# Kernel tuning notes

Measured on AMD Instinct MI355X. Metric: run time of the kernel, lower is better.

## Reference

```python
import jax, jax.numpy as jnp
import numpy as np

T, B, F, H = 128, 64, 75, 512
J = F  # attention dim == number of input features (joints)


def _lstm_dir(x, h0, c0, Wih, Whh, bih, bhh, reverse):
    # x: (T,B,Fin). Precompute input projection once (big GEMM), scan the recurrence.
    xw = jnp.einsum('tbf,gf->tbg', x, Wih) + bih + bhh  # (T,B,4H)

    def step(carry, xt):
        h, c = carry
        g = xt + h @ Whh.T  # (B,4H), PyTorch gate order i,f,g,o
        i, f, gg, o = jnp.split(g, 4, axis=-1)
        c = jax.nn.sigmoid(f) * c + jax.nn.sigmoid(i) * jnp.tanh(gg)
        h = jax.nn.sigmoid(o) * jnp.tanh(c)
        return (h, c), h

    (hT, cT), ys = jax.lax.scan(step, (h0, c0), xw, reverse=reverse)
    return ys, hT


def _bilstm(x, h0, c0, Wih, Whh, bih, bhh):
    # params have leading direction axis of size 2
    yf, hf = _lstm_dir(x, h0[0], c0[0], Wih[0], Whh[0], bih[0], bhh[0], False)
    yb, hb = _lstm_dir(x, h0[1], c0[1], Wih[1], Whh[1], bih[1], bhh[1], True)
    return jnp.concatenate([yf, yb], axis=-1), jnp.stack([hf, hb])


def setup_inputs() -> dict:
    key = jax.random.key(0)
    ks = iter(jax.random.split(key, 40))

    def p(*shape):
        return (jax.random.normal(next(ks), shape, dtype=jnp.float32) * 0.05)

    inp = {
        'x': jax.random.normal(next(ks), (T, B, F), dtype=jnp.float32),
        'h0': jnp.zeros((6, B, H), jnp.float32),
        'c0': jnp.zeros((6, B, H), jnp.float32),
        # salstm: 1-layer bidirectional, input F
        'sa_Wih': p(2, 4 * H, F), 'sa_Whh': p(2, 4 * H, H),
        'sa_bih': p(2, 4 * H), 'sa_bhh': p(2, 4 * H),
        # mainlstm layer 0 (input F)
        'm0_Wih': p(2, 4 * H, F), 'm0_Whh': p(2, 4 * H, H),
        'm0_bih': p(2, 4 * H), 'm0_bhh': p(2, 4 * H),
        # mainlstm layers 1,2 (input 2H), stacked on leading layer axis
        'mL_Wih': p(2, 2, 4 * H, 2 * H), 'mL_Whh': p(2, 2, 4 * H, H),
        'mL_bih': p(2, 2, 4 * H), 'mL_bhh': p(2, 2, 4 * H),
        'safc1_W': p(H, H), 'safc1_b': p(H),
        'safc2_W': p(J, H), 'safc2_b': p(J),
        'fc1_W': p(H, 2 * H), 'fc1_b': p(H),
    }
    return inp


def reference(x, h0, c0, sa_Wih, sa_Whh, sa_bih, sa_bhh,
              m0_Wih, m0_Whh, m0_bih, m0_bhh,
              mL_Wih, mL_Whh, mL_bih, mL_bhh,
              safc1_W, safc1_b, safc2_W, safc2_b, fc1_W, fc1_b):
    # spatial-attention LSTM
    sa_out, sa_hn = _bilstm(x, h0[:2], c0[:2], sa_Wih, sa_Whh, sa_bih, sa_bhh)  # sa_hn (2,B,H)
    e = jnp.exp(jnp.tanh(sa_hn @ safc1_W.T + safc1_b) @ safc2_W.T + safc2_b)  # (2,B,J)
    alpha = e / e.sum(axis=(0, 2), keepdims=True)  # per-batch normalization
    # replace all weights >= 0.1 with their selected mean (per batch element)
    mask = alpha >= 0.1
    cnt = mask.sum(axis=(0, 2), keepdims=True)
    sel_mean = (alpha * mask).sum(axis=(0, 2), keepdims=True) / jnp.maximum(cnt, 1)
    alpha = jnp.where(mask, sel_mean, alpha)
    alpha_b = alpha.mean(axis=0)  # (B,J) -- reconcile direction axis for broadcast

    xw = x * alpha_b[None]  # (T,B,F)

    # 3-layer bidirectional main LSTM
    y, _ = _bilstm(xw, h0[0:2], c0[0:2], m0_Wih, m0_Whh, m0_bih, m0_bhh)
    for l in range(2):
        y, _ = _bilstm(y, h0[2 + 2 * l:4 + 2 * l], c0[2 + 2 * l:4 + 2 * l],
                       mL_Wih[l], mL_Whh[l], mL_bih[l], mL_bhh[l])
    out = y @ fc1_W.T + fc1_b  # (T,B,H)
    return out
```

## Files before the change

### kernel.cpp

```cpp
#include <hip/hip_runtime.h>
#include <cstddef>

#define T_  128
#define B_  64
#define F_  75
#define H_  512
#define G4_ 2048
#define TB_ (T_ * B_)
#define KP_ 128

typedef __bf16 bf16x8 __attribute__((ext_vector_type(8)));
typedef float  f32x4  __attribute__((ext_vector_type(4)));
typedef unsigned long long u64;

__device__ __forceinline__ short f2b(float x) {
    union { float f; unsigned u; } v; v.f = x;
    return (short)((v.u + 0x7fffu + ((v.u >> 16) & 1u)) >> 16);
}
__device__ __forceinline__ float b2f(short s) {
    union { float f; unsigned u; } v; v.u = ((unsigned)(unsigned short)s) << 16;
    return v.f;
}
__device__ __forceinline__ void gload16(const void* g, void* l) {
    __builtin_amdgcn_global_load_lds(
        (const __attribute__((address_space(1))) void*)g,
        (__attribute__((address_space(3))) void*)l, 16, 0, 0);
}
__device__ __forceinline__ float fsig(float x) {
    return __builtin_amdgcn_rcpf(1.f + __expf(-x));
}
__device__ __forceinline__ float ftanh(float x) {
    return 1.f - 2.f * __builtin_amdgcn_rcpf(1.f + __expf(2.f * x));
}

__global__ __launch_bounds__(256) void gemm_bf16(
    const short* __restrict__ A, const short* __restrict__ Bm,
    float* __restrict__ C, float* __restrict__ P, int M, int N, int K,
    const float* __restrict__ bias1, const float* __restrict__ bias2)
{
    __shared__ short As[4096];
    __shared__ short Bs[4096];
    const int tid = threadIdx.x;
    const int m_base = blockIdx.y * 128;
    const int n_base = blockIdx.x * 128;
    const int w = tid >> 6, lane = tid & 63;
    const int wm = (w >> 1) * 64, wn = (w & 1) * 64;
    const int lm = lane & 15, q = lane >> 4;

    f32x4 acc[4][4];
#pragma unroll
    for (int i = 0; i < 4; i++)
#pragma unroll
        for (int j = 0; j < 4; j++)
#pragma unroll
            for (int r = 0; r < 4; r++) acc[i][j][r] = 0.f;

    const int s0 = tid, s1 = tid + 256;
    const int r0 = s0 & 127, c0 = s0 >> 7;
    const int r1 = s1 & 127, c1 = s1 >> 7;

    for (int k0 = 0; k0 < K; k0 += 32) {
        __syncthreads();
        gload16(A + (size_t)(m_base + r0) * K + k0 + c0 * 8, &As[s0 * 8]);
        gload16(A + (size_t)(m_base + r1) * K + k0 + c1 * 8, &As[s1 * 8]);
        gload16(Bm + (size_t)(n_base + r0) * K + k0 + c0 * 8, &Bs[s0 * 8]);
        gload16(Bm + (size_t)(n_base + r1) * K + k0 + c1 * 8, &Bs[s1 * 8]);
        __syncthreads();
        bf16x8 af[4], bfv[4];
#pragma unroll
        for (int i = 0; i < 4; i++) {
            af[i]  = *(const bf16x8*)&As[((q * 128) + wm + i * 16 + lm) * 8];
            bfv[i] = *(const bf16x8*)&Bs[((q * 128) + wn + i * 16 + lm) * 8];
        }
#pragma unroll
        for (int i = 0; i < 4; i++)
#pragma unroll
            for (int j = 0; j < 4; j++)
                acc[i][j] = __builtin_amdgcn_mfma_f32_16x16x32_bf16(
                    af[i], bfv[j], acc[i][j], 0, 0, 0);
    }

#pragma unroll
    for (int i = 0; i < 4; i++) {
#pragma unroll
        for (int j = 0; j < 4; j++) {
            const int gm0 = m_base + wm + i * 16 + q * 4;
            const int gn = n_base + wn + j * 16 + lm;
            float bb = (bias1 ? bias1[gn] : 0.f) + (bias2 ? bias2[gn] : 0.f);
            if (P) {
                const int g = gn >> 9, u = gn & 511;
                const int ub = u >> 4, lmu = u & 15;
#pragma unroll
                for (int r = 0; r < 4; r++) {
                    const int gm = gm0 + r;
                    const int t = gm >> 6, b = gm & 63;
                    const int tidS = (b >> 4) * 64 + ((b >> 2) & 3) * 16 + lmu;
                    size_t idx = ((((size_t)t * 32 + ub) * 4 + (b & 3)) * 256 + tidS) * 4 + g;
                    P[idx] = acc[i][j][r] + bb;
                }
            } else {
#pragma unroll
                for (int r = 0; r < 4; r++)
                    C[(size_t)(gm0 + r) * N + gn] = acc[i][j][r] + bb;
            }
        }
    }
}

__global__ __launch_bounds__(256) void pack_whh(
    const float* __restrict__ W, short* __restrict__ Wpk)
{
    int i = blockIdx.x * 256 + threadIdx.x;
    if (i >= 2 * G4_ * H_) return;
    int e = i & 7, lane = (i >> 3) & 63, it = (i >> 9) & 15;
    int g = (i >> 13) & 3, ub = (i >> 15) & 31, dir = (i >> 20) & 1;
    int lm = lane & 15, qq = lane >> 4;
    float v = W[((size_t)dir * G4_ + g * H_ + ub * 16 + lm) * H_
                + it * 32 + qq * 8 + e];
    Wpk[i] = f2b(v);
}

__global__ __launch_bounds__(256) void init_phase(
    const float* __restrict__ h0s, short* __restrict__ Ht,
    unsigned* __restrict__ bar, int zero_bar)
{
    int i = blockIdx.x * 256 + threadIdx.x;
    if (i < 2 * B_ * H_) Ht[i] = f2b(h0s[i]);
    if (zero_bar && i < 64) bar[i] = 0;
}

__global__ __launch_bounds__(256) void ht_to_f32(
    const short* __restrict__ Ht0, float* __restrict__ out)
{
    int i = blockIdx.x * 256 + threadIdx.x;
    if (i < 2 * B_ * H_) out[i] = b2f(Ht0[i]);
}

__global__ __launch_bounds__(256, 1) void lstm_phase(
    const float* __restrict__ XW,
    const short* __restrict__ Wpk,
    short* __restrict__ Ht,
    const float* __restrict__ c0p,
    short* __restrict__ Y,
    unsigned* __restrict__ bar, int phase)
{
    __shared__ short Ws[32768];
    __shared__ short Tb[64 * 24];
    const int dir = blockIdx.y, ub = blockIdx.x, u0 = ub * 16;
    const int tid = threadIdx.x, w = tid >> 6, lane = tid & 63;
    const int lm = lane & 15, q = lane >> 4;

    const short* wsrc = Wpk + (size_t)(dir * 32 + ub) * 32768;
#pragma unroll
    for (int p = 0; p < 16; p++)
        gload16(wsrc + (tid + 256 * p) * 8, &Ws[(tid + 256 * p) * 8]);

    const int b0 = w * 16 + q * 4;
    const int u = u0 + lm;
    unsigned* slots = bar + dir * 32;

    float c[4];
    f32x4 xw[4];
#pragma unroll
    for (int r = 0; r < 4; r++)
        c[r] = c0p[(size_t)dir * B_ * H_ + (size_t)(b0 + r) * H_ + u];
    {
        const int t0 = dir ? (T_ - 1) : 0;
        const float* xp = XW + ((size_t)dir * T_ + t0) * (B_ * G4_) + (size_t)ub * 4096;
#pragma unroll
        for (int r = 0; r < 4; r++)
            xw[r] = *(const f32x4*)(xp + r * 1024 + tid * 4);
    }
    __syncthreads();

    for (int s = 0; s < T_; s++) {
        const int t = dir ? (T_ - 1 - s) : s;
        const short* Hc = Ht + ((size_t)((s & 1) * 2 + dir) << 15);

        u64 hq[32];
#pragma unroll
        for (int it = 0; it < 16; it++) {
            const u64* hp = (const u64*)(Hc + (w * 16 + lm) * 512 + it * 32 + q * 8);
            hq[2 * it]     = __hip_atomic_load((u64*)hp,     __ATOMIC_RELAXED, __HIP_MEMORY_SCOPE_AGENT);
            hq[2 * it + 1] = __hip_atomic_load((u64*)hp + 1, __ATOMIC_RELAXED, __HIP_MEMORY_SCOPE_AGENT);
        }

        f32x4 acc[4];
#pragma unroll
        for (int g = 0; g < 4; g++)
#pragma unroll
            for (int r = 0; r < 4; r++) acc[g][r] = 0.f;

#pragma unroll
        for (int it = 0; it < 16; it++) {
            union { u64 q2[2]; bf16x8 v; } ua;
            ua.q2[0] = hq[2 * it]; ua.q2[1] = hq[2 * it + 1];
#pragma unroll
            for (int g = 0; g < 4; g++) {
                bf16x8 bv = *(const bf16x8*)&Ws[((g * 16 + it) * 64 + lane) * 8];
                acc[g] = __builtin_amdgcn_mfma_f32_16x16x32_bf16(ua.v, bv, acc[g], 0, 0, 0);
            }
        }

#pragma unroll
        for (int r = 0; r < 4; r++) {
            float gi = acc[0][r] + xw[r][0];
            float gf = acc[1][r] + xw[r][1];
            float gg = acc[2][r] + xw[r][2];
            float go = acc[3][r] + xw[r][3];
            float cc = fsig(gf) * c[r] + fsig(gi) * ftanh(gg);
            c[r] = cc;
            Tb[(b0 + r) * 24 + lm] = f2b(fsig(go) * ftanh(cc));
        }
        __syncthreads();

        {
            const int b = tid >> 2, qd = tid & 3;
            u64 v0 = *(const u64*)&Tb[b * 24 + qd * 4];
            short* Hn = Ht + ((size_t)(((s + 1) & 1) * 2 + dir) << 15);
            __hip_atomic_store((u64*)(Hn + b * 512 + u0 + qd * 4), v0,
                               __ATOMIC_RELAXED, __HIP_MEMORY_SCOPE_AGENT);
            if (Y)
                *(u64*)(Y + ((size_t)t * B_ + b) * (2 * H_) + dir * H_ + u0 + qd * 4) = v0;
        }
        __asm__ volatile("s_waitcnt vmcnt(0)" ::: "memory");

        const unsigned tgt4 = (unsigned)(phase * T_ + s + 1) * 4u;
        if (lane == 0)
            __hip_atomic_fetch_add(&slots[ub], 1u, __ATOMIC_RELAXED, __HIP_MEMORY_SCOPE_AGENT);

        if (s < T_ - 1) {
            const int tn = dir ? (T_ - 2 - s) : (s + 1);
            const float* xp = XW + ((size_t)dir * T_ + tn) * (B_ * G4_) + (size_t)ub * 4096;
#pragma unroll
            for (int r = 0; r < 4; r++)
                xw[r] = *(const f32x4*)(xp + r * 1024 + tid * 4);
        }

        unsigned v;
        do {
            __builtin_amdgcn_s_sleep(1);
            v = (lane < 32)
                ? __hip_atomic_load(&slots[lane], __ATOMIC_RELAXED, __HIP_MEMORY_SCOPE_AGENT)
                : tgt4;
        } while (__any(v < tgt4));
        __syncthreads();
    }
}

__global__ __launch_bounds__(256) void gemm_bt(
    const float* __restrict__ A, const float* __restrict__ Bm,
    float* __restrict__ C, int M, int N, int K,
    const float* __restrict__ bias1, int act)
{
    __shared__ float As[16][68];
    __shared__ float Bs[16][68];
    const int tid = threadIdx.x;
    const int m_base = blockIdx.y * 64;
    const int n_base = blockIdx.x * 64;
    const int tm = tid >> 4, tn = tid & 15;
    float acc[4][4] = {};

    for (int k0 = 0; k0 < K; k0 += 16) {
#pragma unroll
        for (int i = 0; i < 4; i++) {
            int idx = tid * 4 + i;
            int r = idx >> 4, kk = idx & 15;
            int gm = m_base + r, gk = k0 + kk;
            As[kk][r] = (gm < M && gk < K) ? A[(size_t)gm * K + gk] : 0.f;
            int gn = n_base + r;
            Bs[kk][r] = (gn < N && gk < K) ? Bm[(size_t)gn * K + gk] : 0.f;
        }
        __syncthreads();
#pragma unroll
        for (int kk = 0; kk < 16; kk++) {
            float4 av = *(const float4*)&As[kk][tm * 4];
            float4 bv = *(const float4*)&Bs[kk][tn * 4];
            float a[4] = {av.x, av.y, av.z, av.w};
            float b[4] = {bv.x, bv.y, bv.z, bv.w};
#pragma unroll
            for (int i = 0; i < 4; i++)
#pragma unroll
                for (int j = 0; j < 4; j++)
                    acc[i][j] = fmaf(a[i], b[j], acc[i][j]);
        }
        __syncthreads();
    }
#pragma unroll
    for (int i = 0; i < 4; i++) {
        int gm = m_base + tm * 4 + i;
        if (gm >= M) continue;
#pragma unroll
        for (int j = 0; j < 4; j++) {
            int gn = n_base + tn * 4 + j;
            if (gn >= N) continue;
            float v = acc[i][j];
            if (bias1) v += bias1[gn];
            if (act == 1) v = tanhf(v);
            else if (act == 2) v = expf(v);
            C[(size_t)gm * N + gn] = v;
        }
    }
}

__global__ __launch_bounds__(256) void conv_f2b(
    const float* __restrict__ src, short* __restrict__ dst, int n)
{
    int i = blockIdx.x * 256 + threadIdx.x;
    if (i < n) dst[i] = f2b(src[i]);
}
__global__ __launch_bounds__(256) void conv_f2b_pad(
    const float* __restrict__ src, short* __restrict__ dst,
    int rows, int kin, int kp)
{
    int i = blockIdx.x * 256 + threadIdx.x;
    if (i < rows * kp) {
        int r = i / kp, k = i % kp;
        dst[i] = (k < kin) ? f2b(src[(size_t)r * kin + k]) : (short)0;
    }
}

__global__ __launch_bounds__(256) void attn_alpha(
    const float* __restrict__ E, float* __restrict__ AB)
{
    const int b = blockIdx.x, tid = threadIdx.x;
    __shared__ float red[256];
    __shared__ float adj[152];
    float v = 0.f;
    if (tid < 150) {
        int d = tid / F_, j = tid % F_;
        v = E[((size_t)d * B_ + b) * F_ + j];
    }
    red[tid] = v; __syncthreads();
    for (int s2 = 128; s2 > 0; s2 >>= 1) {
        if (tid < s2) red[tid] += red[tid + s2];
        __syncthreads();
    }
    float total = red[0]; __syncthreads();
    float alpha = v / total;
    float m = (tid < 150 && alpha >= 0.1f) ? 1.f : 0.f;
    red[tid] = m; __syncthreads();
    for (int s2 = 128; s2 > 0; s2 >>= 1) {
        if (tid < s2) red[tid] += red[tid + s2];
        __syncthreads();
    }
    float cnt = red[0]; __syncthreads();
    red[tid] = m * alpha; __syncthreads();
    for (int s2 = 128; s2 > 0; s2 >>= 1) {
        if (tid < s2) red[tid] += red[tid + s2];
        __syncthreads();
    }
    float selsum = red[0]; __syncthreads();
    float selmean = selsum / fmaxf(cnt, 1.f);
    if (tid < 150) adj[tid] = (m > 0.f) ? selmean : alpha;
    __syncthreads();
    if (tid < F_) AB[(size_t)b * F_ + tid] = 0.5f * (adj[tid] + adj[F_ + tid]);
}

__global__ __launch_bounds__(256) void scale_xb(
    const float* __restrict__ x, const float* __restrict__ AB,
    short* __restrict__ xb)
{
    int i = blockIdx.x * 256 + threadIdx.x;
    if (i < TB_ * KP_) {
        int r = i >> 7, k = i & 127;
        if (k < F_) {
            int b = r % B_;
            xb[i] = f2b(x[(size_t)r * F_ + k] * AB[(size_t)b * F_ + k]);
        } else xb[i] = 0;
    }
}

extern "C" void kernel_launch(void* const* d_in, const int* in_sizes, int n_in,
                              void* d_out, int out_size, void* d_ws, size_t ws_size,
                              hipStream_t stream)
{
    (void)in_sizes; (void)n_in; (void)out_size; (void)ws_size;
    const float* x       = (const float*)d_in[0];
    const float* h0      = (const float*)d_in[1];
    const float* c0      = (const float*)d_in[2];
    const float* sa_Wih  = (const float*)d_in[3];
    const float* sa_Whh  = (const float*)d_in[4];
    const float* sa_bih  = (const float*)d_in[5];
    const float* sa_bhh  = (const float*)d_in[6];
    const float* m0_Wih  = (const float*)d_in[7];
    const float* m0_Whh  = (const float*)d_in[8];
    const float* m0_bih  = (const float*)d_in[9];
    const float* m0_bhh  = (const float*)d_in[10];
    const float* mL_Wih  = (const float*)d_in[11];
    const float* mL_Whh  = (const float*)d_in[12];
    const float* mL_bih  = (const float*)d_in[13];
    const float* mL_bhh  = (const float*)d_in[14];
    const float* safc1_W = (const float*)d_in[15];
    const float* safc1_b = (const float*)d_in[16];
    const float* safc2_W = (const float*)d_in[17];
    const float* safc2_b = (const float*)d_in[18];
    const float* fc1_W   = (const float*)d_in[19];
    const float* fc1_b   = (const float*)d_in[20];

    char* cur = (char*)d_ws;
    auto alloc = [&](size_t bytes) {
        char* p = cur; cur += (bytes + 255) & ~(size_t)255; return p;
    };
    float*    XW   = (float*)alloc((size_t)2 * TB_ * G4_ * 4);
    float*    T1b  = (float*)alloc(2 * B_ * H_ * 4);
    float*    Eb   = (float*)alloc(2 * B_ * F_ * 4);
    float*    AB   = (float*)alloc(B_ * F_ * 4);
    float*    saHf = (float*)alloc(2 * B_ * H_ * 4);
    short*    xb   = (short*)alloc((size_t)TB_ * KP_ * 2);
    short*    Y0b  = (short*)alloc((size_t)TB_ * 2 * H_ * 2);
    short*    Y1b  = (short*)alloc((size_t)TB_ * 2 * H_ * 2);
    short*    Ht   = (short*)alloc((size_t)2 * 2 * B_ * H_ * 2);
    short*    Wpk  = (short*)alloc((size_t)2 * G4_ * H_ * 2);
    short*    Wihb = (short*)alloc((size_t)2 * G4_ * KP_ * 2);
    short*    WihbL= (short*)alloc((size_t)2 * G4_ * 2 * H_ * 2);
    short*    fc1b = (short*)alloc((size_t)H_ * 2 * H_ * 2);
    unsigned* bar  = (unsigned*)alloc(256);

    auto cv = [&](const float* s, short* d, int n) {
        conv_f2b<<<(n + 255) / 256, 256, 0, stream>>>(s, d, n);
    };
    auto g16 = [&](const short* Ap, const short* Bp, float* Cp, float* Pp,
                   int M, int N, int K, const float* b1, const float* b2) {
        gemm_bf16<<<dim3(N / 128, M / 128), 256, 0, stream>>>(Ap, Bp, Cp, Pp, M, N, K, b1, b2);
    };
    auto phase = [&](const float* Whh_p, const float* h0p, const float* c0p,
                     short* Yout, int pidx) {
        pack_whh<<<(2 * G4_ * H_ + 255) / 256, 256, 0, stream>>>(Whh_p, Wpk);
        init_phase<<<256, 256, 0, stream>>>(h0p, Ht, bar, pidx == 0 ? 1 : 0);
        lstm_phase<<<dim3(32, 2), 256, 0, stream>>>(XW, Wpk, Ht, c0p, Yout, bar, pidx);
    };

    cv(fc1_W, fc1b, H_ * 2 * H_);

    conv_f2b_pad<<<(TB_ * KP_ + 255) / 256, 256, 0, stream>>>(x, xb, TB_, F_, KP_);
    conv_f2b_pad<<<(2 * G4_ * KP_ + 255) / 256, 256, 0, stream>>>(sa_Wih, Wihb, 2 * G4_, F_, KP_);
    for (int d = 0; d < 2; d++)
        g16(xb, Wihb + (size_t)d * G4_ * KP_, nullptr, XW + (size_t)d * TB_ * G4_,
            TB_, G4_, KP_, sa_bih + d * G4_, sa_bhh + d * G4_);
    phase(sa_Whh, h0, c0, nullptr, 0);
    ht_to_f32<<<256, 256, 0, stream>>>(Ht, saHf);
    gemm_bt<<<dim3(8, 2), 256, 0, stream>>>(saHf, safc1_W, T1b, 2 * B_, H_, H_, safc1_b, 1);
    gemm_bt<<<dim3(2, 2), 256, 0, stream>>>(T1b, safc2_W, Eb, 2 * B_, F_, H_, safc2_b, 2);
    attn_alpha<<<B_, 256, 0, stream>>>(Eb, AB);
    scale_xb<<<(TB_ * KP_ + 255) / 256, 256, 0, stream>>>(x, AB, xb);

    conv_f2b_pad<<<(2 * G4_ * KP_ + 255) / 256, 256, 0, stream>>>(m0_Wih, Wihb, 2 * G4_, F_, KP_);
    for (int d = 0; d < 2; d++)
        g16(xb, Wihb + (size_t)d * G4_ * KP_, nullptr, XW + (size_t)d * TB_ * G4_,
            TB_, G4_, KP_, m0_bih + d * G4_, m0_bhh + d * G4_);
    phase(m0_Whh, h0, c0, Y0b, 1);

    cv(mL_Wih, WihbL, 2 * G4_ * 2 * H_);
    for (int d = 0; d < 2; d++)
        g16(Y0b, WihbL + (size_t)d * G4_ * 2 * H_, nullptr, XW + (size_t)d * TB_ * G4_,
            TB_, G4_, 2 * H_, mL_bih + d * G4_, mL_bhh + d * G4_);
    phase(mL_Whh, h0 + 2 * B_ * H_, c0 + 2 * B_ * H_, Y1b, 2);

    cv(mL_Wih + (size_t)2 * G4_ * 2 * H_, WihbL, 2 * G4_ * 2 * H_);
    for (int d = 0; d < 2; d++)
        g16(Y1b, WihbL + (size_t)d * G4_ * 2 * H_, nullptr, XW + (size_t)d * TB_ * G4_,
            TB_, G4_, 2 * H_, mL_bih + (2 + d) * G4_, mL_bhh + (2 + d) * G4_);
    phase(mL_Whh + (size_t)2 * G4_ * H_, h0 + 4 * B_ * H_, c0 + 4 * B_ * H_, Y0b, 3);

    g16(Y0b, fc1b, (float*)d_out, nullptr, TB_, H_, 2 * H_, fc1_b, nullptr);
}
```

Baseline: 4.214 ms.

## Replace per-step grid barrier with sentinel-based dataflow polling on hidden sequence

The global per-timestep barrier (atomic counters plus spin) is replaced by writing each step's hidden state directly into a full-sequence buffer pre-filled with 0xFFFF sentinels. Consumer blocks poll their own needed h elements until no sentinel remains, so only the true data dependency is waited on. The separate Y write and the double-buffered Ht are removed, and a memset per phase is added. This relies on 0xFFFF (a bf16 NaN) never being a legitimate output and on store visibility ordering, and it risks stale reads of the Tb buffer without a trailing syncthreads, even though Tb is now double-buffered.

After: 4.463 ms. 1.06x slower.

```diff
diff --git a/kernel.cpp b/kernel.cpp
--- a/kernel.cpp
+++ b/kernel.cpp
@@ -31,6 +31,12 @@
 }
 __device__ __forceinline__ float ftanh(float x) {
     return 1.f - 2.f * __builtin_amdgcn_rcpf(1.f + __expf(2.f * x));
+}
+__device__ __forceinline__ u64 aload(const u64* p) {
+    return __hip_atomic_load(p, __ATOMIC_RELAXED, __HIP_MEMORY_SCOPE_AGENT);
+}
+__device__ __forceinline__ void astore(u64* p, u64 v) {
+    __hip_atomic_store(p, v, __ATOMIC_RELAXED, __HIP_MEMORY_SCOPE_AGENT);
 }
 
 __global__ __launch_bounds__(256) void gemm_bf16(
@@ -121,31 +127,32 @@
 }
 
 __global__ __launch_bounds__(256) void init_phase(
-    const float* __restrict__ h0s, short* __restrict__ Ht,
-    unsigned* __restrict__ bar, int zero_bar)
-{
-    int i = blockIdx.x * 256 + threadIdx.x;
-    if (i < 2 * B_ * H_) Ht[i] = f2b(h0s[i]);
-    if (zero_bar && i < 64) bar[i] = 0;
-}
-
-__global__ __launch_bounds__(256) void ht_to_f32(
-    const short* __restrict__ Ht0, float* __restrict__ out)
-{
-    int i = blockIdx.x * 256 + threadIdx.x;
-    if (i < 2 * B_ * H_) out[i] = b2f(Ht0[i]);
+    const float* __restrict__ h0s, short* __restrict__ Ht0)
+{
+    int i = blockIdx.x * 256 + threadIdx.x;
+    if (i < 2 * B_ * H_) Ht0[i] = f2b(h0s[i]);
+}
+
+__global__ __launch_bounds__(256) void extract_sahf(
+    const short* __restrict__ Hseq, float* __restrict__ out)
+{
+    int i = blockIdx.x * 256 + threadIdx.x;
+    if (i < 2 * B_ * H_) {
+        int u = i & 511, b = (i >> 9) & 63, dir = i >> 15;
+        int t = dir ? 0 : (T_ - 1);
+        out[i] = b2f(Hseq[((size_t)t * B_ + b) * 1024 + dir * 512 + u]);
+    }
 }
 
 __global__ __launch_bounds__(256, 1) void lstm_phase(
     const float* __restrict__ XW,
     const short* __restrict__ Wpk,
-    short* __restrict__ Ht,
-    const float* __restrict__ c0p,
-    short* __restrict__ Y,
-    unsigned* __restrict__ bar, int phase)
+    const short* __restrict__ Ht0,
+    short* __restrict__ Hseq,
+    const float* __restrict__ c0p)
 {
     __shared__ short Ws[32768];
-    __shared__ short Tb[64 * 24];
+    __shared__ short Tb[2][64 * 24];
     const int dir = blockIdx.y, ub = blockIdx.x, u0 = ub * 16;
     const int tid = threadIdx.x, w = tid >> 6, lane = tid & 63;
     const int lm = lane & 15, q = lane >> 4;
@@ -156,40 +163,58 @@
         gload16(wsrc + (tid + 256 * p) * 8, &Ws[(tid + 256 * p) * 8]);
 
     const int b0 = w * 16 + q * 4;
+    const int r = w * 16 + lm;
     const int u = u0 + lm;
-    unsigned* slots = bar + dir * 32;
 
     float c[4];
     f32x4 xw[4];
 #pragma unroll
-    for (int r = 0; r < 4; r++)
-        c[r] = c0p[(size_t)dir * B_ * H_ + (size_t)(b0 + r) * H_ + u];
+    for (int rr = 0; rr < 4; rr++)
+        c[rr] = c0p[(size_t)dir * B_ * H_ + (size_t)(b0 + rr) * H_ + u];
     {
         const int t0 = dir ? (T_ - 1) : 0;
         const float* xp = XW + ((size_t)dir * T_ + t0) * (B_ * G4_) + (size_t)ub * 4096;
 #pragma unroll
-        for (int r = 0; r < 4; r++)
-            xw[r] = *(const f32x4*)(xp + r * 1024 + tid * 4);
+        for (int rr = 0; rr < 4; rr++)
+            xw[rr] = *(const f32x4*)(xp + rr * 1024 + tid * 4);
     }
     __syncthreads();
 
     for (int s = 0; s < T_; s++) {
         const int t = dir ? (T_ - 1 - s) : s;
-        const short* Hc = Ht + ((size_t)((s & 1) * 2 + dir) << 15);
+        const int tp = dir ? (T_ - s) : (s - 1);
+        const short* hrow = (s == 0)
+            ? (Ht0 + ((size_t)dir * B_ + r) * 512)
+            : (Hseq + ((size_t)tp * B_ + r) * 1024 + dir * 512);
 
         u64 hq[32];
 #pragma unroll
         for (int it = 0; it < 16; it++) {
-            const u64* hp = (const u64*)(Hc + (w * 16 + lm) * 512 + it * 32 + q * 8);
-            hq[2 * it]     = __hip_atomic_load((u64*)hp,     __ATOMIC_RELAXED, __HIP_MEMORY_SCOPE_AGENT);
-            hq[2 * it + 1] = __hip_atomic_load((u64*)hp + 1, __ATOMIC_RELAXED, __HIP_MEMORY_SCOPE_AGENT);
+            const u64* hp = (const u64*)(hrow + it * 32 + q * 8);
+            hq[2 * it]     = aload(hp);
+            hq[2 * it + 1] = aload(hp + 1);
+        }
+        if (s > 0) {
+            int tries = 0;
+            while (true) {
+                bool stale = false;
+#pragma unroll
+                for (int j = 0; j < 32; j++)
+                    stale |= ((unsigned)hq[j] & 0xFFFFu) == 0xFFFFu;
+                if (!__any(stale) || ++tries > (1 << 16)) break;
+                __builtin_amdgcn_s_sleep(1);
+#pragma unroll
+                for (int j = 0; j < 32; j++)
+                    if (((unsigned)hq[j] & 0xFFFFu) == 0xFFFFu)
+                        hq[j] = aload((const u64*)(hrow + (j >> 1) * 32 + q * 8) + (j & 1));
+            }
         }
 
         f32x4 acc[4];
 #pragma unroll
         for (int g = 0; g < 4; g++)
 #pragma unroll
-            for (int r = 0; r < 4; r++) acc[g][r] = 0.f;
+            for (int rr = 0; rr < 4; rr++) acc[g][rr] = 0.f;
 
 #pragma unroll
         for (int it = 0; it < 16; it++) {
@@ -202,49 +227,32 @@
             }
         }
 
-#pragma unroll
-        for (int r = 0; r < 4; r++) {
-            float gi = acc[0][r] + xw[r][0];
-            float gf = acc[1][r] + xw[r][1];
-            float gg = acc[2][r] + xw[r][2];
-            float go = acc[3][r] + xw[r][3];
-            float cc = fsig(gf) * c[r] + fsig(gi) * ftanh(gg);
-            c[r] = cc;
-            Tb[(b0 + r) * 24 + lm] = f2b(fsig(go) * ftanh(cc));
+        short* tb = Tb[s & 1];
+#pragma unroll
+        for (int rr = 0; rr < 4; rr++) {
+            float gi = acc[0][rr] + xw[rr][0];
+            float gf = acc[1][rr] + xw[rr][1];
+            float gg = acc[2][rr] + xw[rr][2];
+            float go = acc[3][rr] + xw[rr][3];
+            float cc = fsig(gf) * c[rr] + fsig(gi) * ftanh(gg);
+            c[rr] = cc;
+            tb[(b0 + rr) * 24 + lm] = f2b(fsig(go) * ftanh(cc));
         }
         __syncthreads();
 
         {
             const int b = tid >> 2, qd = tid & 3;
-            u64 v0 = *(const u64*)&Tb[b * 24 + qd * 4];
-            short* Hn = Ht + ((size_t)(((s + 1) & 1) * 2 + dir) << 15);
-            __hip_atomic_store((u64*)(Hn + b * 512 + u0 + qd * 4), v0,
-                               __ATOMIC_RELAXED, __HIP_MEMORY_SCOPE_AGENT);
-            if (Y)
-                *(u64*)(Y + ((size_t)t * B_ + b) * (2 * H_) + dir * H_ + u0 + qd * 4) = v0;
-        }
-        __asm__ volatile("s_waitcnt vmcnt(0)" ::: "memory");
-
-        const unsigned tgt4 = (unsigned)(phase * T_ + s + 1) * 4u;
-        if (lane == 0)
-            __hip_atomic_fetch_add(&slots[ub], 1u, __ATOMIC_RELAXED, __HIP_MEMORY_SCOPE_AGENT);
+            u64 v0 = *(const u64*)&tb[b * 24 + qd * 4];
+            astore((u64*)(Hseq + ((size_t)t * B_ + b) * 1024 + dir * 512 + u0 + qd * 4), v0);
+        }
 
         if (s < T_ - 1) {
             const int tn = dir ? (T_ - 2 - s) : (s + 1);
             const float* xp = XW + ((size_t)dir * T_ + tn) * (B_ * G4_) + (size_t)ub * 4096;
 #pragma unroll
-            for (int r = 0; r < 4; r++)
-                xw[r] = *(const f32x4*)(xp + r * 1024 + tid * 4);
-        }
-
-        unsigned v;
-        do {
-            __builtin_amdgcn_s_sleep(1);
-            v = (lane < 32)
-                ? __hip_atomic_load(&slots[lane], __ATOMIC_RELAXED, __HIP_MEMORY_SCOPE_AGENT)
-                : tgt4;
-        } while (__any(v < tgt4));
-        __syncthreads();
+            for (int rr = 0; rr < 4; rr++)
+                xw[rr] = *(const f32x4*)(xp + rr * 1024 + tid * 4);
+        }
     }
 }
 
@@ -265,11 +273,11 @@
 #pragma unroll
         for (int i = 0; i < 4; i++) {
             int idx = tid * 4 + i;
-            int r = idx >> 4, kk = idx & 15;
-            int gm = m_base + r, gk = k0 + kk;
-            As[kk][r] = (gm < M && gk < K) ? A[(size_t)gm * K + gk] : 0.f;
-            int gn = n_base + r;
-            Bs[kk][r] = (gn < N && gk < K) ? Bm[(size_t)gn * K + gk] : 0.f;
+            int rr = idx >> 4, kk = idx & 15;
+            int gm = m_base + rr, gk = k0 + kk;
+            As[kk][rr] = (gm < M && gk < K) ? A[(size_t)gm * K + gk] : 0.f;
+            int gn = n_base + rr;
+            Bs[kk][rr] = (gn < N && gk < K) ? Bm[(size_t)gn * K + gk] : 0.f;
         }
         __syncthreads();
 #pragma unroll
@@ -315,8 +323,8 @@
 {
     int i = blockIdx.x * 256 + threadIdx.x;
     if (i < rows * kp) {
-        int r = i / kp, k = i % kp;
-        dst[i] = (k < kin) ? f2b(src[(size_t)r * kin + k]) : (short)0;
+        int rr = i / kp, k = i % kp;
+        dst[i] = (k < kin) ? f2b(src[(size_t)rr * kin + k]) : (short)0;
     }
 }
 
@@ -363,10 +371,10 @@
 {
     int i = blockIdx.x * 256 + threadIdx.x;
     if (i < TB_ * KP_) {
-        int r = i >> 7, k = i & 127;
+        int rr = i >> 7, k = i & 127;
         if (k < F_) {
-            int b = r % B_;
-            xb[i] = f2b(x[(size_t)r * F_ + k] * AB[(size_t)b * F_ + k]);
+            int b = rr % B_;
+            xb[i] = f2b(x[(size_t)rr * F_ + k] * AB[(size_t)b * F_ + k]);
         } else xb[i] = 0;
     }
 }
@@ -402,20 +410,21 @@
     auto alloc = [&](size_t bytes) {
         char* p = cur; cur += (bytes + 255) & ~(size_t)255; return p;
     };
+    const size_t YB = (size_t)TB_ * 2 * H_ * 2;
     float*    XW   = (float*)alloc((size_t)2 * TB_ * G4_ * 4);
     float*    T1b  = (float*)alloc(2 * B_ * H_ * 4);
     float*    Eb   = (float*)alloc(2 * B_ * F_ * 4);
     float*    AB   = (float*)alloc(B_ * F_ * 4);
     float*    saHf = (float*)alloc(2 * B_ * H_ * 4);
     short*    xb   = (short*)alloc((size_t)TB_ * KP_ * 2);
-    short*    Y0b  = (short*)alloc((size_t)TB_ * 2 * H_ * 2);
-    short*    Y1b  = (short*)alloc((size_t)TB_ * 2 * H_ * 2);
-    short*    Ht   = (short*)alloc((size_t)2 * 2 * B_ * H_ * 2);
+    short*    HsA  = (short*)alloc(YB);
+    short*    Y0b  = (short*)alloc(YB);
+    short*    Y1b  = (short*)alloc(YB);
+    short*    Ht0  = (short*)alloc(2 * B_ * H_ * 2);
     short*    Wpk  = (short*)alloc((size_t)2 * G4_ * H_ * 2);
     short*    Wihb = (short*)alloc((size_t)2 * G4_ * KP_ * 2);
     short*    WihbL= (short*)alloc((size_t)2 * G4_ * 2 * H_ * 2);
     short*    fc1b = (short*)alloc((size_t)H_ * 2 * H_ * 2);
-    unsigned* bar  = (unsigned*)alloc(256);
 
     auto cv = [&](const float* s, short* d, int n) {
         conv_f2b<<<(n + 255) / 256, 256, 0, stream>>>(s, d, n);
@@ -425,10 +434,11 @@
         gemm_bf16<<<dim3(N / 128, M / 128), 256, 0, stream>>>(Ap, Bp, Cp, Pp, M, N, K, b1, b2);
     };
     auto phase = [&](const float* Whh_p, const float* h0p, const float* c0p,
-                     short* Yout, int pidx) {
+                     short* Hseq) {
         pack_whh<<<(2 * G4_ * H_ + 255) / 256, 256, 0, stream>>>(Whh_p, Wpk);
-        init_phase<<<256, 256, 0, stream>>>(h0p, Ht, bar, pidx == 0 ? 1 : 0);
-        lstm_phase<<<dim3(32, 2), 256, 0, stream>>>(XW, Wpk, Ht, c0p, Yout, bar, pidx);
+        init_phase<<<256, 256, 0, stream>>>(h0p, Ht0);
+        hipMemsetAsync(Hseq, 0xFF, YB, stream);
+        lstm_phase<<<dim3(32, 2), 256, 0, stream>>>(XW, Wpk, Ht0, Hseq, c0p);
     };
 
     cv(fc1_W, fc1b, H_ * 2 * H_);
@@ -438,8 +448,8 @@
     for (int d = 0; d < 2; d++)
         g16(xb, Wihb + (size_t)d * G4_ * KP_, nullptr, XW + (size_t)d * TB_ * G4_,
             TB_, G4_, KP_, sa_bih + d * G4_, sa_bhh + d * G4_);
-    phase(sa_Whh, h0, c0, nullptr, 0);
-    ht_to_f32<<<256, 256, 0, stream>>>(Ht, saHf);
+    phase(sa_Whh, h0, c0, HsA);
+    extract_sahf<<<256, 256, 0, stream>>>(HsA, saHf);
     gemm_bt<<<dim3(8, 2), 256, 0, stream>>>(saHf, safc1_W, T1b, 2 * B_, H_, H_, safc1_b, 1);
     gemm_bt<<<dim3(2, 2), 256, 0, stream>>>(T1b, safc2_W, Eb, 2 * B_, F_, H_, safc2_b, 2);
     attn_alpha<<<B_, 256, 0, stream>>>(Eb, AB);
@@ -449,19 +459,19 @@
     for (int d = 0; d < 2; d++)
         g16(xb, Wihb + (size_t)d * G4_ * KP_, nullptr, XW + (size_t)d * TB_ * G4_,
             TB_, G4_, KP_, m0_bih + d * G4_, m0_bhh + d * G4_);
-    phase(m0_Whh, h0, c0, Y0b, 1);
+    phase(m0_Whh, h0, c0, Y0b);
 
     cv(mL_Wih, WihbL, 2 * G4_ * 2 * H_);
     for (int d = 0; d < 2; d++)
         g16(Y0b, WihbL + (size_t)d * G4_ * 2 * H_, nullptr, XW + (size_t)d * TB_ * G4_,
             TB_, G4_, 2 * H_, mL_bih + d * G4_, mL_bhh + d * G4_);
-    phase(mL_Whh, h0 + 2 * B_ * H_, c0 + 2 * B_ * H_, Y1b, 2);
+    phase(mL_Whh, h0 + 2 * B_ * H_, c0 + 2 * B_ * H_, Y1b);
 
     cv(mL_Wih + (size_t)2 * G4_ * 2 * H_, WihbL, 2 * G4_ * 2 * H_);
     for (int d = 0; d < 2; d++)
         g16(Y1b, WihbL + (size_t)d * G4_ * 2 * H_, nullptr, XW + (size_t)d * TB_ * G4_,
             TB_, G4_, 2 * H_, mL_bih + (2 + d) * G4_, mL_bhh + (2 + d) * G4_);
-    phase(mL_Whh + (size_t)2 * G4_ * H_, h0 + 4 * B_ * H_, c0 + 4 * B_ * H_, Y0b, 3);
+    phase(mL_Whh + (size_t)2 * G4_ * H_, h0 + 4 * B_ * H_, c0 + 4 * B_ * H_, Y0b);
 
     g16(Y0b, fc1b, (float*)d_out, nullptr, TB_, H_, 2 * H_, fc1_b, nullptr);
 }
```
